# Optimization experiments

Measured on AMD Instinct MI355X. Metric: run time of the kernel, lower is better.

Reference implementation:

```python
import jax, jax.numpy as jnp
import numpy as np

N = 50000      # nodes
E = 800000     # edges
D_IN = 128     # embedding_in
EP = 200000    # prediction edge pairs
CONV_DIMS = [D_IN, 128, 64, 32]
LIN_DIMS = [32, 16, 8, 1]


def setup_inputs() -> dict:
    key = jax.random.key(0)
    ks = jax.random.split(key, 20)
    inp = {
        "x": jax.random.normal(ks[0], (N, D_IN), dtype=jnp.float32),
        "edge_index": jax.random.randint(ks[1], (2, E), 0, N, dtype=jnp.int64 if jax.config.jax_enable_x64 else jnp.int32),
        "pred_edges": jax.random.randint(ks[2], (EP, 2), 0, N, dtype=jnp.int64 if jax.config.jax_enable_x64 else jnp.int32),
    }
    k = 3
    for i in range(3):  # GCNConv weights [in,out] + bias (torch GCNConv has bias)
        din, dout = CONV_DIMS[i], CONV_DIMS[i + 1]
        inp[f"cw{i}"] = jax.random.normal(ks[k], (din, dout), dtype=jnp.float32) / np.sqrt(din); k += 1
        inp[f"cb{i}"] = jax.random.normal(ks[k], (dout,), dtype=jnp.float32) * 0.01; k += 1
    for i in range(3):  # Linear weights stored [in,out]
        din, dout = LIN_DIMS[i], LIN_DIMS[i + 1]
        inp[f"lw{i}"] = jax.random.normal(ks[k], (din, dout), dtype=jnp.float32) / np.sqrt(din); k += 1
        inp[f"lb{i}"] = jax.random.normal(ks[k], (dout,), dtype=jnp.float32) * 0.01; k += 1
    return inp


def gcn_conv(x, W, b, src, dst, n):
    """PyG GCNConv: D^-1/2 (A + I) D^-1/2 X W + b, deg over dst incl. self-loop."""
    h = x @ W  # [n, dout]
    deg = jax.ops.segment_sum(jnp.ones_like(dst, dtype=h.dtype), dst, num_segments=n) + 1.0
    dis = jax.lax.rsqrt(deg)  # deg >= 1 (self loop)
    msg = h[src] * (dis[src] * dis[dst])[:, None]      # gather + per-edge normalize
    out = jax.ops.segment_sum(msg, dst, num_segments=n)  # scatter-add into targets
    out = out + h * (dis * dis)[:, None]                # self-loop contribution
    return out + b


def reference(x, edge_index, pred_edges, cw0, cb0, cw1, cb1, cw2, cb2,
              lw0, lb0, lw1, lb1, lw2, lb2):
    src, dst = edge_index[0], edge_index[1]
    n = x.shape[0]
    for W, b in ((cw0, cb0), (cw1, cb1), (cw2, cb2)):
        x = jax.nn.relu(gcn_conv(x, W, b, src, dst, n))
    x = jax.nn.relu(x @ lw0 + lb0)
    x = jax.nn.relu(x @ lw1 + lb1)
    x = jax.nn.sigmoid(x @ lw2 + lb2)  # [n, 1]
    s = x[:, 0]
    # x[pred_edges] -> [EP,2,1]; mul of pair, transpose+flatten -> [EP]
    return s[pred_edges[:, 0]] * s[pred_edges[:, 1]]
```

## Files before the change

kernel.cpp:

```cpp
#include <hip/hip_runtime.h>
#include <math.h>

constexpr int NN  = 50000;
constexpr int NP  = 50048;
constexpr int NE  = 800000;
constexpr int NEP = 200000;

constexpr int NBKT  = 256;
constexpr int CAP   = 4096;
constexpr int CAPC  = 4096;
constexpr int CHUNK = 4096;

constexpr int BKB = (NE + CHUNK - 1) / CHUNK;
constexpr int W0B = 128 * 128 / 256;
constexpr int W1B = 128 * 64 / 256;
constexpr int W2B = 64 * 32 / 256;
constexpr int FRONT_BLOCKS = BKB + W0B + W1B + W2B;

constexpr int NODE_BLKS32 = (NN + 31) / 32;
constexpr int NODE_BLKS16 = (NN + 15) / 16;

typedef _Float16 half8_t __attribute__((ext_vector_type(8)));
typedef float    float4_t __attribute__((ext_vector_type(4)));

static inline int cdiv(long long a, int b) { return (int)((a + b - 1) / b); }

__global__ __launch_bounds__(256) void k_front(const int* __restrict__ src,
        const int* __restrict__ dst, int* __restrict__ binCnt,
        unsigned int* __restrict__ ebuf,
        const float* __restrict__ cw0, _Float16* __restrict__ WT0,
        const float* __restrict__ cw1, _Float16* __restrict__ WT1,
        const float* __restrict__ cw2, _Float16* __restrict__ WT2) {
    const int tid = threadIdx.x;
    const int bid = blockIdx.x;

    if (bid < BKB) {
        __shared__ int hist[NBKT];
        __shared__ int base[NBKT];
        __shared__ int cur[NBKT];
        constexpr int J = CHUNK / 256;
        const int e0 = bid * CHUNK;
        hist[tid] = 0;
        __syncthreads();
        int  s[J], bn[J], dl[J];
        bool ok[J];
#pragma unroll
        for (int j = 0; j < J; ++j) {
            int i = e0 + j * 256 + tid;
            ok[j] = i < NE;
            if (ok[j]) {
                int d = dst[i];
                s[j]  = src[i];
                bn[j] = d >> 8;
                dl[j] = d & 255;
                atomicAdd(&hist[bn[j]], 1);
            }
        }
        __syncthreads();
        base[tid] = hist[tid] ? atomicAdd(&binCnt[tid], hist[tid]) : 0;
        cur[tid] = 0;
        __syncthreads();
#pragma unroll
        for (int j = 0; j < J; ++j) {
            if (ok[j]) {
                int slot = base[bn[j]] + atomicAdd(&cur[bn[j]], 1);
                ebuf[bn[j] * CAP + slot] = (unsigned int)s[j] | ((unsigned int)dl[j] << 16);
            }
        }
        return;
    }
    if (bid < BKB + W0B) {
        int idx = (bid - BKB) * 256 + tid;
        int k = idx >> 7, n = idx & 127;
        WT0[(size_t)n * 128 + k] = (_Float16)cw0[idx];
        return;
    }
    if (bid < BKB + W0B + W1B) {
        int idx = (bid - BKB - W0B) * 256 + tid;
        int k = idx >> 6, n = idx & 63;
        WT1[(size_t)n * 128 + k] = (_Float16)cw1[idx];
        return;
    }
    {
        int idx = (bid - BKB - W0B - W1B) * 256 + tid;
        int k = idx >> 5, n = idx & 31;
        WT2[(size_t)n * 64 + k] = (_Float16)cw2[idx];
    }
}

__global__ __launch_bounds__(256) void k_csrbuild(const unsigned int* __restrict__ ebuf,
        const int* __restrict__ binCnt, int* __restrict__ off, float* __restrict__ dis,
        unsigned short* __restrict__ csr) {
    __shared__ int hist[256];
    __shared__ int sh[256];
    __shared__ int cur[256];
    const int tid = threadIdx.x;
    const int bin = blockIdx.x;
    const int cnt = binCnt[bin];
    const unsigned int* eb = ebuf + (size_t)bin * CAP;

    hist[tid] = 0;
    __syncthreads();
    for (int i = tid; i < cnt; i += 256)
        atomicAdd(&hist[eb[i] >> 16], 1);
    __syncthreads();

    int v  = hist[tid];
    int pv = (v + 3) & ~3;
    sh[tid] = pv;
    __syncthreads();
    for (int d = 1; d < 256; d <<= 1) {
        int t = (tid >= d) ? sh[tid - d] : 0;
        __syncthreads();
        sh[tid] += t;
        __syncthreads();
    }
    int start = bin * CAPC + (sh[tid] - pv);

    int node = bin * 256 + tid;
    if (node < NN) {
        off[node] = start | (pv << 20);
        dis[node] = rsqrtf((float)v + 1.0f);
    }
    cur[tid] = start;
    __syncthreads();

    for (int i = tid; i < cnt; i += 256) {
        unsigned int e = eb[i];
        int p = atomicAdd(&cur[e >> 16], 1);
        csr[p] = (unsigned short)(e & 0xFFFFu);
    }
    for (int k2 = v; k2 < pv; ++k2) csr[start + k2] = (unsigned short)NN;
}

__global__ __launch_bounds__(256) void k_gemm0(const float* __restrict__ X,
        const _Float16* __restrict__ WT, const float* __restrict__ dis,
        _Float16* __restrict__ g, int n) {
    constexpr int K = 128, DOUT = 128;
    constexpr int NC = 64, NT = 4, KT = 4, MT = 2;

    const int tid  = threadIdx.x;
    const int L    = tid & 63;
    const int w    = tid >> 6;
    const int wc   = w & 1;
    const int wr   = w >> 1;
    const int r0   = blockIdx.x * 64 + wr * 32;
    const int c0   = wc * NC;
    const int quad = L >> 4;
    const int lm   = L & 15;

    float4_t acc[MT][NT];
#pragma unroll
    for (int mt = 0; mt < MT; ++mt)
#pragma unroll
        for (int nt = 0; nt < NT; ++nt) acc[mt][nt] = (float4_t){0.f, 0.f, 0.f, 0.f};

#pragma unroll
    for (int kt = 0; kt < KT; ++kt) {
        half8_t a[MT], b[NT];
#pragma unroll
        for (int mt = 0; mt < MT; ++mt) {
            const float* xr = X + (size_t)(r0 + mt * 16 + lm) * K + kt * 32 + quad * 8;
            float4 u = *(const float4*)xr;
            float4 v = *(const float4*)(xr + 4);
            a[mt] = (half8_t){(_Float16)u.x, (_Float16)u.y, (_Float16)u.z, (_Float16)u.w,
                              (_Float16)v.x, (_Float16)v.y, (_Float16)v.z, (_Float16)v.w};
        }
#pragma unroll
        for (int nt = 0; nt < NT; ++nt)
            b[nt] = *(const half8_t*)(WT + (size_t)(c0 + nt * 16 + lm) * K + kt * 32 + quad * 8);
#pragma unroll
        for (int mt = 0; mt < MT; ++mt)
#pragma unroll
            for (int nt = 0; nt < NT; ++nt)
                acc[mt][nt] = __builtin_amdgcn_mfma_f32_16x16x32_f16(a[mt], b[nt], acc[mt][nt], 0, 0, 0);
    }

#pragma unroll
    for (int mt = 0; mt < MT; ++mt) {
        int rb = r0 + mt * 16 + quad * 4;
        float dv[4];
        *(float4*)dv = *(const float4*)(dis + rb);
#pragma unroll
        for (int nt = 0; nt < NT; ++nt) {
            int c = c0 + nt * 16 + lm;
#pragma unroll
            for (int reg = 0; reg < 4; ++reg) {
                int r = rb + reg;
                if (r < n)       g[(size_t)r * DOUT + c] = (_Float16)(acc[mt][nt][reg] * dv[reg]);
                else if (r == n) g[(size_t)r * DOUT + c] = (_Float16)0.f;
            }
        }
    }
}

__global__ __launch_bounds__(256) void k_agg_gemm16(const half8_t* __restrict__ gin,
        const float* __restrict__ dis, const float* __restrict__ bias,
        const int* __restrict__ off, const unsigned short* __restrict__ csr,
        const _Float16* __restrict__ WT, _Float16* __restrict__ gout, int n) {
    constexpr int DIN = 128, DOUT = 64;
    constexpr int R8 = DIN / 8;
    constexpr int XS = DIN + 8;
    __shared__ _Float16 sX[16 * XS];

    const int tid  = threadIdx.x;
    const int l16  = tid & 15;
    const int ln   = tid >> 4;
    const int r0   = blockIdx.x * 16;
    const int node = r0 + ln;

    if (blockIdx.x == 0 && tid < DOUT / 8)
        ((half8_t*)(gout + (size_t)n * DOUT))[tid] =
            (half8_t){(_Float16)0.f, (_Float16)0.f, (_Float16)0.f, (_Float16)0.f,
                      (_Float16)0.f, (_Float16)0.f, (_Float16)0.f, (_Float16)0.f};

    float dd = dis[node];
    half8_t hv = gin[(size_t)node * R8 + l16];
    float a[8];
#pragma unroll
    for (int j = 0; j < 8; ++j) a[j] = (float)hv[j];

    int pk = off[node];
    int e0 = pk & 0xFFFFF;
    int e1 = e0 + (pk >> 20);
    int e = e0;
    for (; e + 7 < e1; e += 8) {
        ushort4 c4 = *(const ushort4*)(csr + e);
        ushort4 c8 = *(const ushort4*)(csr + e + 4);
        half8_t v0 = gin[(size_t)c4.x * R8 + l16];
        half8_t v1 = gin[(size_t)c4.y * R8 + l16];
        half8_t v2 = gin[(size_t)c4.z * R8 + l16];
        half8_t v3 = gin[(size_t)c4.w * R8 + l16];
        half8_t v4 = gin[(size_t)c8.x * R8 + l16];
        half8_t v5 = gin[(size_t)c8.y * R8 + l16];
        half8_t v6 = gin[(size_t)c8.z * R8 + l16];
        half8_t v7 = gin[(size_t)c8.w * R8 + l16];
#pragma unroll
        for (int j = 0; j < 8; ++j)
            a[j] += ((float)v0[j] + (float)v1[j]) + ((float)v2[j] + (float)v3[j])
                  + ((float)v4[j] + (float)v5[j]) + ((float)v6[j] + (float)v7[j]);
    }
    if (e < e1) {
        ushort4 c4 = *(const ushort4*)(csr + e);
        half8_t v0 = gin[(size_t)c4.x * R8 + l16];
        half8_t v1 = gin[(size_t)c4.y * R8 + l16];
        half8_t v2 = gin[(size_t)c4.z * R8 + l16];
        half8_t v3 = gin[(size_t)c4.w * R8 + l16];
#pragma unroll
        for (int j = 0; j < 8; ++j)
            a[j] += ((float)v0[j] + (float)v1[j]) + ((float)v2[j] + (float)v3[j]);
    }
    {
        half8_t o;
#pragma unroll
        for (int j = 0; j < 8; ++j)
            o[j] = (_Float16)fmaxf(fmaf(a[j], dd, bias[l16 * 8 + j]), 0.f);
        *(half8_t*)(sX + ln * XS + l16 * 8) = o;
    }
    __syncthreads();

    const int L    = tid & 63;
    const int w    = tid >> 6;
    const int quad = L >> 4;
    const int lm   = L & 15;
    const int c0   = w * 16;

    float4_t acc = (float4_t){0.f, 0.f, 0.f, 0.f};
#pragma unroll
    for (int kt = 0; kt < DIN / 32; ++kt) {
        half8_t b  = *(const half8_t*)(WT + (size_t)(c0 + lm) * DIN + kt * 32 + quad * 8);
        half8_t aF = *(const half8_t*)(sX + lm * XS + kt * 32 + quad * 8);
        acc = __builtin_amdgcn_mfma_f32_16x16x32_f16(aF, b, acc, 0, 0, 0);
    }
    int rb = r0 + quad * 4;
    float dv[4];
    *(float4*)dv = *(const float4*)(dis + rb);
#pragma unroll
    for (int reg = 0; reg < 4; ++reg)
        gout[(size_t)(rb + reg) * DOUT + c0 + lm] = (_Float16)(acc[reg] * dv[reg]);
}

__global__ __launch_bounds__(256) void k_agg_gemm8(const half8_t* __restrict__ gin,
        const float* __restrict__ dis, const float* __restrict__ bias,
        const int* __restrict__ off, const unsigned short* __restrict__ csr,
        const _Float16* __restrict__ WT, _Float16* __restrict__ gout, int n) {
    constexpr int DIN = 64, DOUT = 32;
    constexpr int R8 = DIN / 8;
    constexpr int XS = DIN + 8;
    __shared__ _Float16 sX[32 * XS];

    const int tid  = threadIdx.x;
    const int l8   = tid & 7;
    const int ln   = tid >> 3;
    const int r0   = blockIdx.x * 32;
    const int node = r0 + ln;

    if (node < n) {
        float dd = dis[node];
        half8_t hv = gin[(size_t)node * R8 + l8];
        float a[8];
#pragma unroll
        for (int j = 0; j < 8; ++j) a[j] = (float)hv[j];
        int pk = off[node];
        int e0 = pk & 0xFFFFF;
        int e1 = e0 + (pk >> 20);
        int e = e0;
        for (; e + 7 < e1; e += 8) {
            ushort4 c4 = *(const ushort4*)(csr + e);
            ushort4 c8 = *(const ushort4*)(csr + e + 4);
            half8_t v0 = gin[(size_t)c4.x * R8 + l8];
            half8_t v1 = gin[(size_t)c4.y * R8 + l8];
            half8_t v2 = gin[(size_t)c4.z * R8 + l8];
            half8_t v3 = gin[(size_t)c4.w * R8 + l8];
            half8_t v4 = gin[(size_t)c8.x * R8 + l8];
            half8_t v5 = gin[(size_t)c8.y * R8 + l8];
            half8_t v6 = gin[(size_t)c8.z * R8 + l8];
            half8_t v7 = gin[(size_t)c8.w * R8 + l8];
#pragma unroll
            for (int j = 0; j < 8; ++j)
                a[j] += ((float)v0[j] + (float)v1[j]) + ((float)v2[j] + (float)v3[j])
                      + ((float)v4[j] + (float)v5[j]) + ((float)v6[j] + (float)v7[j]);
        }
        if (e < e1) {
            ushort4 c4 = *(const ushort4*)(csr + e);
            half8_t v0 = gin[(size_t)c4.x * R8 + l8];
            half8_t v1 = gin[(size_t)c4.y * R8 + l8];
            half8_t v2 = gin[(size_t)c4.z * R8 + l8];
            half8_t v3 = gin[(size_t)c4.w * R8 + l8];
#pragma unroll
            for (int j = 0; j < 8; ++j)
                a[j] += ((float)v0[j] + (float)v1[j]) + ((float)v2[j] + (float)v3[j]);
        }
        half8_t o;
#pragma unroll
        for (int j = 0; j < 8; ++j)
            o[j] = (_Float16)fmaxf(fmaf(a[j], dd, bias[l8 * 8 + j]), 0.f);
        *(half8_t*)(sX + ln * XS + l8 * 8) = o;
    } else {
        *(half8_t*)(sX + ln * XS + l8 * 8) =
            (half8_t){(_Float16)0.f, (_Float16)0.f, (_Float16)0.f, (_Float16)0.f,
                      (_Float16)0.f, (_Float16)0.f, (_Float16)0.f, (_Float16)0.f};
    }
    __syncthreads();

    const int L    = tid & 63;
    const int w    = tid >> 6;
    const int quad = L >> 4;
    const int lm   = L & 15;
    const int c0   = (w & 1) * 16;
    const int m0   = (w >> 1) * 16;

    float4_t acc = (float4_t){0.f, 0.f, 0.f, 0.f};
#pragma unroll
    for (int kt = 0; kt < DIN / 32; ++kt) {
        half8_t b  = *(const half8_t*)(WT + (size_t)(c0 + lm) * DIN + kt * 32 + quad * 8);
        half8_t aF = *(const half8_t*)(sX + (m0 + lm) * XS + kt * 32 + quad * 8);
        acc = __builtin_amdgcn_mfma_f32_16x16x32_f16(aF, b, acc, 0, 0, 0);
    }
    int rb = r0 + m0 + quad * 4;
    float dv[4];
    *(float4*)dv = *(const float4*)(dis + rb);
#pragma unroll
    for (int reg = 0; reg < 4; ++reg) {
        int r = rb + reg;
        if (r < n)       gout[(size_t)r * DOUT + c0 + lm] = (_Float16)(acc[reg] * dv[reg]);
        else if (r == n) gout[(size_t)r * DOUT + c0 + lm] = (_Float16)0.f;
    }
}

__global__ __launch_bounds__(256) void k_agg_mlp(const half8_t* __restrict__ g,
        const float* __restrict__ dis, const float* __restrict__ b,
        const int* __restrict__ off, const unsigned short* __restrict__ csr,
        const float* __restrict__ lw0, const float* __restrict__ lb0,
        const float* __restrict__ lw1, const float* __restrict__ lb1,
        const float* __restrict__ lw2, const float* __restrict__ lb2,
        float* __restrict__ sv, int n) {
    __shared__ float sh[32 * 33];
    const int tid  = threadIdx.x;
    const int l8   = tid & 7;
    const int lane = l8 & 3;
    const int grp  = l8 >> 2;
    const int ln   = tid >> 3;
    const int node = blockIdx.x * 32 + ln;

    if (node < n) {
        float dd = dis[node];
        half8_t hv = g[(size_t)node * 4 + lane];
        float a[8];
#pragma unroll
        for (int j = 0; j < 8; ++j) a[j] = (grp == 0) ? (float)hv[j] : 0.f;
        int pk = off[node];
        int e0 = pk & 0xFFFFF;
        int e1 = e0 + (pk >> 20);
        for (int e = e0 + grp * 4; e < e1; e += 8) {
            ushort4 c4 = *(const ushort4*)(csr + e);
            half8_t v0 = g[(size_t)c4.x * 4 + lane];
            half8_t v1 = g[(size_t)c4.y * 4 + lane];
            half8_t v2 = g[(size_t)c4.z * 4 + lane];
            half8_t v3 = g[(size_t)c4.w * 4 + lane];
#pragma unroll
            for (int j = 0; j < 8; ++j)
                a[j] += (float)v0[j] + (float)v1[j] + (float)v2[j] + (float)v3[j];
        }
#pragma unroll
        for (int j = 0; j < 8; ++j) a[j] += __shfl_xor(a[j], 4);
        if (grp == 0) {
            float* row = sh + ln * 33 + lane * 8;
#pragma unroll
            for (int j = 0; j < 8; ++j)
                row[j] = fmaxf(fmaf(a[j], dd, b[lane * 8 + j]), 0.f);
        }
    }
    __syncthreads();

    if (tid < 32) {
        int node2 = blockIdx.x * 32 + tid;
        if (node2 < n) {
            const float* v = sh + tid * 33;
            float a[16];
#pragma unroll
            for (int j = 0; j < 16; ++j) {
                float acc = lb0[j];
#pragma unroll
                for (int k = 0; k < 32; ++k) acc = fmaf(v[k], lw0[k * 16 + j], acc);
                a[j] = fmaxf(acc, 0.f);
            }
            float b8[8];
#pragma unroll
            for (int j = 0; j < 8; ++j) {
                float acc = lb1[j];
#pragma unroll
                for (int k = 0; k < 16; ++k) acc = fmaf(a[k], lw1[k * 8 + j], acc);
                b8[j] = fmaxf(acc, 0.f);
            }
            float z = lb2[0];
#pragma unroll
            for (int k = 0; k < 8; ++k) z = fmaf(b8[k], lw2[k], z);
            sv[node2] = 1.0f / (1.0f + expf(-z));
        }
    }
}

__global__ void k_pred(const float* __restrict__ s, const int* __restrict__ pe,
                       float* __restrict__ out, int ep2) {
    int i = blockIdx.x * blockDim.x + threadIdx.x;
    if (i >= ep2) return;
    int4 p = ((const int4*)pe)[i];
    float2 o;
    o.x = s[p.x] * s[p.y];
    o.y = s[p.z] * s[p.w];
    ((float2*)out)[i] = o;
}

extern "C" void kernel_launch(void* const* d_in, const int* in_sizes, int n_in,
                              void* d_out, int out_size, void* d_ws, size_t ws_size,
                              hipStream_t stream) {
    const float* x   = (const float*)d_in[0];
    const int*   ei  = (const int*)d_in[1];
    const int*   pe  = (const int*)d_in[2];
    const float* cw0 = (const float*)d_in[3];
    const float* cb0 = (const float*)d_in[4];
    const float* cw1 = (const float*)d_in[5];
    const float* cb1 = (const float*)d_in[6];
    const float* cw2 = (const float*)d_in[7];
    const float* cb2 = (const float*)d_in[8];
    const float* lw0 = (const float*)d_in[9];
    const float* lb0 = (const float*)d_in[10];
    const float* lw1 = (const float*)d_in[11];
    const float* lb1 = (const float*)d_in[12];
    const float* lw2 = (const float*)d_in[13];
    const float* lb2 = (const float*)d_in[14];

    const int* src = ei;
    const int* dst = ei + NE;

    char* w = (char*)d_ws;
    float*          dis  = (float*)w;           w += sizeof(float) * NN;
    _Float16*       M0   = (_Float16*)w;        w += sizeof(_Float16) * (size_t)(NN + 1) * 128;
    _Float16*       M1   = (_Float16*)w;        w += sizeof(_Float16) * (size_t)(NN + 1) * 64;
    _Float16*       M2   = (_Float16*)w;        w += sizeof(_Float16) * (size_t)(NN + 1) * 32;
    float*          sv   = (float*)w;           w += sizeof(float) * NN;
    _Float16*       WT0  = (_Float16*)w;        w += sizeof(_Float16) * 128 * 128;
    _Float16*       WT1  = (_Float16*)w;        w += sizeof(_Float16) * 64 * 128;
    _Float16*       WT2  = (_Float16*)w;        w += sizeof(_Float16) * 32 * 64;
    int*            off  = (int*)w;             w += sizeof(int) * NN;
    unsigned short* csr  = (unsigned short*)w;  w += sizeof(unsigned short) * (size_t)NBKT * CAPC;
    int*            binCnt = (int*)w;           w += sizeof(int) * NBKT;
    unsigned int*   ebuf = (unsigned int*)w;    w += sizeof(unsigned int) * (size_t)NBKT * CAP;

    const int T = 256;

    hipMemsetAsync(binCnt, 0, sizeof(int) * NBKT, stream);
    k_front<<<FRONT_BLOCKS, 256, 0, stream>>>(src, dst, binCnt, ebuf,
                                              cw0, WT0, cw1, WT1, cw2, WT2);

    k_csrbuild<<<NBKT, 256, 0, stream>>>(ebuf, binCnt, off, dis, csr);

    k_gemm0<<<NP / 64, 256, 0, stream>>>(x, WT0, dis, M0, NN);

    k_agg_gemm16<<<NODE_BLKS16, 256, 0, stream>>>((const half8_t*)M0, dis, cb0,
                                                  off, csr, WT1, M1, NN);

    k_agg_gemm8<<<NODE_BLKS32, 256, 0, stream>>>((const half8_t*)M1, dis, cb1,
                                                 off, csr, WT2, M2, NN);

    k_agg_mlp<<<NODE_BLKS32, 256, 0, stream>>>((const half8_t*)M2, dis, cb2, off, csr,
                                               lw0, lb0, lw1, lb1, lw2, lb2, sv, NN);

    k_pred<<<cdiv(NEP / 2, T), T, 0, stream>>>(sv, pe, (float*)d_out, NEP / 2);
}
```

Before: 214.3 us.

## Fuse CSR build with first GEMM by moving source normalization into aggregation

The layer-0 GEMM no longer scales rows by dis, which removes its dependency on the CSR build, so both are merged into one launch with disjoint block ranges. The aggregation kernel now applies dis[src] per gathered neighbor with an fma chain, and dis[NN] is set to zero for the padding node. The X conversion also switches to packed round-toward-zero f16 conversions. The trade is one fewer kernel launch and overlap of the CSR build with the GEMM, against extra scattered dis loads per edge in the first aggregation and slightly different rounding.

```diff
diff --git a/kernel.cpp b/kernel.cpp
--- a/kernel.cpp
+++ b/kernel.cpp
@@ -17,10 +17,12 @@
 constexpr int W2B = 64 * 32 / 256;
 constexpr int FRONT_BLOCKS = BKB + W0B + W1B + W2B;
 
+constexpr int GEMM0_BLKS = NP / 64;
 constexpr int NODE_BLKS32 = (NN + 31) / 32;
 constexpr int NODE_BLKS16 = (NN + 15) / 16;
 
-typedef _Float16 half8_t __attribute__((ext_vector_type(8)));
+typedef _Float16 half8_t  __attribute__((ext_vector_type(8)));
+typedef __fp16   fp16x2_t __attribute__((ext_vector_type(2)));
 typedef float    float4_t __attribute__((ext_vector_type(4)));
 
 static inline int cdiv(long long a, int b) { return (int)((a + b - 1) / b); }
@@ -88,63 +90,68 @@
     }
 }
 
-__global__ __launch_bounds__(256) void k_csrbuild(const unsigned int* __restrict__ ebuf,
+__global__ __launch_bounds__(256) void k_csr_gemm0(const unsigned int* __restrict__ ebuf,
         const int* __restrict__ binCnt, int* __restrict__ off, float* __restrict__ dis,
-        unsigned short* __restrict__ csr) {
-    __shared__ int hist[256];
-    __shared__ int sh[256];
-    __shared__ int cur[256];
+        unsigned short* __restrict__ csr,
+        const float* __restrict__ X, const _Float16* __restrict__ WT,
+        _Float16* __restrict__ g, int n) {
     const int tid = threadIdx.x;
-    const int bin = blockIdx.x;
-    const int cnt = binCnt[bin];
-    const unsigned int* eb = ebuf + (size_t)bin * CAP;
-
-    hist[tid] = 0;
-    __syncthreads();
-    for (int i = tid; i < cnt; i += 256)
-        atomicAdd(&hist[eb[i] >> 16], 1);
-    __syncthreads();
-
-    int v  = hist[tid];
-    int pv = (v + 3) & ~3;
-    sh[tid] = pv;
-    __syncthreads();
-    for (int d = 1; d < 256; d <<= 1) {
-        int t = (tid >= d) ? sh[tid - d] : 0;
-        __syncthreads();
-        sh[tid] += t;
-        __syncthreads();
-    }
-    int start = bin * CAPC + (sh[tid] - pv);
-
-    int node = bin * 256 + tid;
-    if (node < NN) {
-        off[node] = start | (pv << 20);
-        dis[node] = rsqrtf((float)v + 1.0f);
-    }
-    cur[tid] = start;
-    __syncthreads();
-
-    for (int i = tid; i < cnt; i += 256) {
-        unsigned int e = eb[i];
-        int p = atomicAdd(&cur[e >> 16], 1);
-        csr[p] = (unsigned short)(e & 0xFFFFu);
-    }
-    for (int k2 = v; k2 < pv; ++k2) csr[start + k2] = (unsigned short)NN;
-}
-
-__global__ __launch_bounds__(256) void k_gemm0(const float* __restrict__ X,
-        const _Float16* __restrict__ WT, const float* __restrict__ dis,
-        _Float16* __restrict__ g, int n) {
+    const int bid = blockIdx.x;
+
+    if (bid < NBKT) {
+        __shared__ int hist[256];
+        __shared__ int sh[256];
+        __shared__ int cur[256];
+        const int bin = bid;
+        const int cnt = binCnt[bin];
+        const unsigned int* eb = ebuf + (size_t)bin * CAP;
+
+        hist[tid] = 0;
+        __syncthreads();
+        for (int i = tid; i < cnt; i += 256)
+            atomicAdd(&hist[eb[i] >> 16], 1);
+        __syncthreads();
+
+        int v  = hist[tid];
+        int pv = (v + 3) & ~3;
+        sh[tid] = pv;
+        __syncthreads();
+        for (int d = 1; d < 256; d <<= 1) {
+            int t = (tid >= d) ? sh[tid - d] : 0;
+            __syncthreads();
+            sh[tid] += t;
+            __syncthreads();
+        }
+        int start = bin * CAPC + (sh[tid] - pv);
+
+        int node = bin * 256 + tid;
+        if (node < NN) {
+            off[node] = start | (pv << 20);
+            dis[node] = rsqrtf((float)v + 1.0f);
+        } else if (node == NN) {
+            dis[node] = 0.f;
+        }
+        cur[tid] = start;
+        __syncthreads();
+
+        for (int i = tid; i < cnt; i += 256) {
+            unsigned int e = eb[i];
+            int p = atomicAdd(&cur[e >> 16], 1);
+            csr[p] = (unsigned short)(e & 0xFFFFu);
+        }
+        for (int k2 = v; k2 < pv; ++k2) csr[start + k2] = (unsigned short)NN;
+        return;
+    }
+
     constexpr int K = 128, DOUT = 128;
     constexpr int NC = 64, NT = 4, KT = 4, MT = 2;
 
-    const int tid  = threadIdx.x;
+    const int gb   = bid - NBKT;
     const int L    = tid & 63;
     const int w    = tid >> 6;
     const int wc   = w & 1;
     const int wr   = w >> 1;
-    const int r0   = blockIdx.x * 64 + wr * 32;
+    const int r0   = gb * 64 + wr * 32;
     const int c0   = wc * NC;
     const int quad = L >> 4;
     const int lm   = L & 15;
@@ -163,8 +170,12 @@
             const float* xr = X + (size_t)(r0 + mt * 16 + lm) * K + kt * 32 + quad * 8;
             float4 u = *(const float4*)xr;
             float4 v = *(const float4*)(xr + 4);
-            a[mt] = (half8_t){(_Float16)u.x, (_Float16)u.y, (_Float16)u.z, (_Float16)u.w,
-                              (_Float16)v.x, (_Float16)v.y, (_Float16)v.z, (_Float16)v.w};
+            union { fp16x2_t h2[4]; half8_t h8; } cv;
+            cv.h2[0] = __builtin_amdgcn_cvt_pkrtz(u.x, u.y);
+            cv.h2[1] = __builtin_amdgcn_cvt_pkrtz(u.z, u.w);
+            cv.h2[2] = __builtin_amdgcn_cvt_pkrtz(v.x, v.y);
+            cv.h2[3] = __builtin_amdgcn_cvt_pkrtz(v.z, v.w);
+            a[mt] = cv.h8;
         }
 #pragma unroll
         for (int nt = 0; nt < NT; ++nt)
@@ -179,15 +190,13 @@
 #pragma unroll
     for (int mt = 0; mt < MT; ++mt) {
         int rb = r0 + mt * 16 + quad * 4;
-        float dv[4];
-        *(float4*)dv = *(const float4*)(dis + rb);
 #pragma unroll
         for (int nt = 0; nt < NT; ++nt) {
             int c = c0 + nt * 16 + lm;
 #pragma unroll
             for (int reg = 0; reg < 4; ++reg) {
                 int r = rb + reg;
-                if (r < n)       g[(size_t)r * DOUT + c] = (_Float16)(acc[mt][nt][reg] * dv[reg]);
+                if (r < n)       g[(size_t)r * DOUT + c] = (_Float16)acc[mt][nt][reg];
                 else if (r == n) g[(size_t)r * DOUT + c] = (_Float16)0.f;
             }
         }
@@ -218,7 +227,7 @@
     half8_t hv = gin[(size_t)node * R8 + l16];
     float a[8];
 #pragma unroll
-    for (int j = 0; j < 8; ++j) a[j] = (float)hv[j];
+    for (int j = 0; j < 8; ++j) a[j] = dd * (float)hv[j];
 
     int pk = off[node];
     int e0 = pk & 0xFFFFF;
@@ -235,10 +244,18 @@
         half8_t v5 = gin[(size_t)c8.y * R8 + l16];
         half8_t v6 = gin[(size_t)c8.z * R8 + l16];
         half8_t v7 = gin[(size_t)c8.w * R8 + l16];
+        float d0 = dis[c4.x], d1 = dis[c4.y], d2 = dis[c4.z], d3 = dis[c4.w];
+        float d4 = dis[c8.x], d5 = dis[c8.y], d6 = dis[c8.z], d7 = dis[c8.w];
 #pragma unroll
         for (int j = 0; j < 8; ++j)
-            a[j] += ((float)v0[j] + (float)v1[j]) + ((float)v2[j] + (float)v3[j])
-                  + ((float)v4[j] + (float)v5[j]) + ((float)v6[j] + (float)v7[j]);
+            a[j] = fmaf((float)v7[j], d7,
+                   fmaf((float)v6[j], d6,
+                   fmaf((float)v5[j], d5,
+                   fmaf((float)v4[j], d4,
+                   fmaf((float)v3[j], d3,
+                   fmaf((float)v2[j], d2,
+                   fmaf((float)v1[j], d1,
+                   fmaf((float)v0[j], d0, a[j]))))))));
     }
     if (e < e1) {
         ushort4 c4 = *(const ushort4*)(csr + e);
@@ -246,9 +263,13 @@
         half8_t v1 = gin[(size_t)c4.y * R8 + l16];
         half8_t v2 = gin[(size_t)c4.z * R8 + l16];
         half8_t v3 = gin[(size_t)c4.w * R8 + l16];
+        float d0 = dis[c4.x], d1 = dis[c4.y], d2 = dis[c4.z], d3 = dis[c4.w];
 #pragma unroll
         for (int j = 0; j < 8; ++j)
-            a[j] += ((float)v0[j] + (float)v1[j]) + ((float)v2[j] + (float)v3[j]);
+            a[j] = fmaf((float)v3[j], d3,
+                   fmaf((float)v2[j], d2,
+                   fmaf((float)v1[j], d1,
+                   fmaf((float)v0[j], d0, a[j]))));
     }
     {
         half8_t o;
@@ -475,7 +496,7 @@
     const int* dst = ei + NE;
 
     char* w = (char*)d_ws;
-    float*          dis  = (float*)w;           w += sizeof(float) * NN;
+    float*          dis  = (float*)w;           w += sizeof(float) * (NN + 16);
     _Float16*       M0   = (_Float16*)w;        w += sizeof(_Float16) * (size_t)(NN + 1) * 128;
     _Float16*       M1   = (_Float16*)w;        w += sizeof(_Float16) * (size_t)(NN + 1) * 64;
     _Float16*       M2   = (_Float16*)w;        w += sizeof(_Float16) * (size_t)(NN + 1) * 32;
@@ -490,13 +511,12 @@
 
     const int T = 256;
 
-    hipMemsetAsync(binCnt, 0, sizeof(int) * NBKT, stream);
+    (void)hipMemsetAsync(binCnt, 0, sizeof(int) * NBKT, stream);
     k_front<<<FRONT_BLOCKS, 256, 0, stream>>>(src, dst, binCnt, ebuf,
                                               cw0, WT0, cw1, WT1, cw2, WT2);
 
-    k_csrbuild<<<NBKT, 256, 0, stream>>>(ebuf, binCnt, off, dis, csr);
-
-    k_gemm0<<<NP / 64, 256, 0, stream>>>(x, WT0, dis, M0, NN);
+    k_csr_gemm0<<<NBKT + GEMM0_BLKS, 256, 0, stream>>>(ebuf, binCnt, off, dis, csr,
+                                                       x, WT0, M0, NN);
 
     k_agg_gemm16<<<NODE_BLKS16, 256, 0, stream>>>((const half8_t*)M0, dis, cb0,
                                                   off, csr, WT1, M1, NN);
```

Result: faster. 199.1 us (-7.1%).
